# Kernel optimization log

Hardware: AMD Instinct MI355X
Metric: run time of the kernel (lower is better)

The kernel has to match this reference:

```python
import jax, jax.numpy as jnp
import numpy as np
import math

N = 100000
C = 128
E = 640000
ALPHA = 0.1
THETA = 1.0
LAYER = 4


def setup_inputs() -> dict:
    key = jax.random.key(0)
    k1, k2, k3, k4, k5, k6 = jax.random.split(key, 6)
    x = jax.random.normal(k1, (N, C), dtype=jnp.float32)
    x0 = jax.random.normal(k2, (N, C), dtype=jnp.float32)
    W = jax.random.normal(k3, (C, C), dtype=jnp.float32) / math.sqrt(C)
    b = jax.random.normal(k4, (C,), dtype=jnp.float32) * 0.01
    edge_index = jax.random.randint(k5, (2, E), 0, N, dtype=jnp.int64)
    return {"x": x, "x0": x0, "W": W, "b": b, "edge_index": edge_index}


def _symmetric_propagate(x, edge_index):
    n = x.shape[0]
    loop = jnp.arange(n, dtype=edge_index.dtype)
    src = jnp.concatenate([edge_index[0], loop])  # add self-loops (GCN norm)
    dst = jnp.concatenate([edge_index[1], loop])
    ones = jnp.ones(src.shape[0], dtype=x.dtype)
    deg = jax.ops.segment_sum(ones, dst, num_segments=n)
    dinv = jnp.where(deg > 0, jax.lax.rsqrt(deg), 0.0)
    norm = dinv[src] * dinv[dst]                  # [E+N]
    msgs = x[src] * norm[:, None]                 # gather + scale
    return jax.ops.segment_sum(msgs, dst, num_segments=n)  # scatter-add


def reference(x, x0, W, b, edge_index):
    propagated = _symmetric_propagate(x, edge_index)
    support = (1.0 - ALPHA) * propagated + ALPHA * x0
    beta = math.log(THETA / max(LAYER, 1) + 1.0)
    transformed = support @ W.T + b               # nn.Linear(channels, channels)
    return (1.0 - beta) * support + beta * transformed
```

## Files before the change

### kernel.cpp

```cpp
#include <hip/hip_runtime.h>
#include <stdint.h>

#define C 128
#define ALPHA_F 0.1f
#define ONE_MINUS_ALPHA 0.9f
#define BETA_F 0.22314355131420976f
#define ONE_MINUS_BETA 0.7768564486857902f
#define KSLOT 16

typedef __attribute__((ext_vector_type(8))) short bf16x8;
typedef __attribute__((ext_vector_type(4))) float f32x4;

__device__ inline float bf2f(unsigned short u) {
    union { unsigned int i; float f; } c;
    c.i = ((unsigned int)u) << 16;
    return c.f;
}
__device__ inline unsigned short f2bf(float f) {
    union { float f; unsigned int i; } c;
    c.f = f;
    unsigned int r = (c.i + 0x7FFFu + ((c.i >> 16) & 1u)) >> 16;
    return (unsigned short)r;
}

__global__ void k_init(const float* __restrict__ W, unsigned short* __restrict__ Vb,
                       int* __restrict__ cnt, int* __restrict__ ovf_cnt, int n) {
    int i = blockIdx.x * 256 + threadIdx.x;
    if (i == 0) *ovf_cnt = 0;
    if (i < n) cnt[i] = 0;
    if (i < C * C) {
        int j = i >> 7;
        int c = i & 127;
        float v = BETA_F * W[i] + ((j == c) ? ONE_MINUS_BETA : 0.f);
        Vb[i] = f2bf(v);
    }
}

__global__ void k_hist_place(const int* __restrict__ src, const int* __restrict__ dst,
                             int* __restrict__ cnt, int* __restrict__ sorted_src,
                             int* __restrict__ ovf_src, int* __restrict__ ovf_dst,
                             int* __restrict__ ovf_cnt, int e) {
    int i = blockIdx.x * blockDim.x + threadIdx.x;
    if (i < e) {
        int d = dst[i];
        int r = atomicAdd(&cnt[d], 1);
        if (r < KSLOT) {
            sorted_src[(size_t)d * KSLOT + r] = src[i];
        } else {
            int p = atomicAdd(ovf_cnt, 1);
            ovf_src[p] = src[i];
            ovf_dst[p] = d;
        }
    }
}

__global__ void k_ybf(const float* __restrict__ x, const int* __restrict__ cnt,
                      unsigned short* __restrict__ y, int n) {
    int t = blockIdx.x * 256 + threadIdx.x;
    int total = n * 32;
    if (t < total) {
        int i = t >> 5;
        float dv = rsqrtf((float)(cnt[i] + 1));
        float4 v = ((const float4*)x)[t];
        ushort4 o;
        o.x = f2bf(v.x * dv);
        o.y = f2bf(v.y * dv);
        o.z = f2bf(v.z * dv);
        o.w = f2bf(v.w * dv);
        ((ushort4*)y)[t] = o;
    }
}

__device__ __forceinline__ float4 acc_node(const ushort4* __restrict__ y4,
                                           int node, int len,
                                           int eidx, int l32, int base) {
    int m = (len < KSLOT) ? len : KSLOT;
    bool b1 = 1 < m, b2 = 2 < m, b3 = 3 < m;
    bool b4 = 4 < m, b5 = 5 < m, b6 = 6 < m, b7 = 7 < m;
    int s0 = __shfl(eidx, base + 0, 64);
    int s1 = __shfl(eidx, base + (b1 ? 1 : 0), 64);
    int s2 = __shfl(eidx, base + (b2 ? 2 : 0), 64);
    int s3 = __shfl(eidx, base + (b3 ? 3 : 0), 64);
    int s4 = __shfl(eidx, base + (b4 ? 4 : 0), 64);
    int s5 = __shfl(eidx, base + (b5 ? 5 : 0), 64);
    int s6 = __shfl(eidx, base + (b6 ? 6 : 0), 64);
    int s7 = __shfl(eidx, base + (b7 ? 7 : 0), 64);
    ushort4 v0 = y4[(size_t)s0 * 32 + l32];
    ushort4 v1 = y4[(size_t)s1 * 32 + l32];
    ushort4 v2 = y4[(size_t)s2 * 32 + l32];
    ushort4 v3 = y4[(size_t)s3 * 32 + l32];
    ushort4 v4 = y4[(size_t)s4 * 32 + l32];
    ushort4 v5 = y4[(size_t)s5 * 32 + l32];
    ushort4 v6 = y4[(size_t)s6 * 32 + l32];
    ushort4 v7 = y4[(size_t)s7 * 32 + l32];
    ushort4 vs = y4[(size_t)node * 32 + l32];

    float w0 = (0 < m) ? 1.f : 0.f, w1 = b1 ? 1.f : 0.f, w2 = b2 ? 1.f : 0.f, w3 = b3 ? 1.f : 0.f;
    float w4 = b4 ? 1.f : 0.f, w5 = b5 ? 1.f : 0.f, w6 = b6 ? 1.f : 0.f, w7 = b7 ? 1.f : 0.f;

    float4 acc;
    acc.x = bf2f(vs.x) + w0 * bf2f(v0.x) + w1 * bf2f(v1.x) + w2 * bf2f(v2.x) + w3 * bf2f(v3.x)
                       + w4 * bf2f(v4.x) + w5 * bf2f(v5.x) + w6 * bf2f(v6.x) + w7 * bf2f(v7.x);
    acc.y = bf2f(vs.y) + w0 * bf2f(v0.y) + w1 * bf2f(v1.y) + w2 * bf2f(v2.y) + w3 * bf2f(v3.y)
                       + w4 * bf2f(v4.y) + w5 * bf2f(v5.y) + w6 * bf2f(v6.y) + w7 * bf2f(v7.y);
    acc.z = bf2f(vs.z) + w0 * bf2f(v0.z) + w1 * bf2f(v1.z) + w2 * bf2f(v2.z) + w3 * bf2f(v3.z)
                       + w4 * bf2f(v4.z) + w5 * bf2f(v5.z) + w6 * bf2f(v6.z) + w7 * bf2f(v7.z);
    acc.w = bf2f(vs.w) + w0 * bf2f(v0.w) + w1 * bf2f(v1.w) + w2 * bf2f(v2.w) + w3 * bf2f(v3.w)
                       + w4 * bf2f(v4.w) + w5 * bf2f(v5.w) + w6 * bf2f(v6.w) + w7 * bf2f(v7.w);

    for (int j = 8; j < m; j += 4) {
        bool c1 = (j + 1) < m, c2 = (j + 2) < m, c3 = (j + 3) < m;
        int t0 = __shfl(eidx, base + j, 64);
        int t1 = __shfl(eidx, base + (c1 ? j + 1 : j), 64);
        int t2 = __shfl(eidx, base + (c2 ? j + 2 : j), 64);
        int t3 = __shfl(eidx, base + (c3 ? j + 3 : j), 64);
        ushort4 u0 = y4[(size_t)t0 * 32 + l32];
        ushort4 u1 = y4[(size_t)t1 * 32 + l32];
        ushort4 u2 = y4[(size_t)t2 * 32 + l32];
        ushort4 u3 = y4[(size_t)t3 * 32 + l32];
        float q1 = c1 ? 1.f : 0.f, q2 = c2 ? 1.f : 0.f, q3 = c3 ? 1.f : 0.f;
        acc.x += bf2f(u0.x) + q1 * bf2f(u1.x) + q2 * bf2f(u2.x) + q3 * bf2f(u3.x);
        acc.y += bf2f(u0.y) + q1 * bf2f(u1.y) + q2 * bf2f(u2.y) + q3 * bf2f(u3.y);
        acc.z += bf2f(u0.z) + q1 * bf2f(u1.z) + q2 * bf2f(u2.z) + q3 * bf2f(u3.z);
        acc.w += bf2f(u0.w) + q1 * bf2f(u1.w) + q2 * bf2f(u2.w) + q3 * bf2f(u3.w);
    }
    return acc;
}

__device__ __forceinline__ float4 add_ovf(float4 acc, const ushort4* __restrict__ y4,
                                          const int* __restrict__ ovf_src,
                                          const int* __restrict__ ovf_dst,
                                          int oc, int node, int l32) {
    for (int j = 0; j < oc; ++j) {
        if (ovf_dst[j] == node) {
            ushort4 u = y4[(size_t)ovf_src[j] * 32 + l32];
            acc.x += bf2f(u.x);
            acc.y += bf2f(u.y);
            acc.z += bf2f(u.z);
            acc.w += bf2f(u.w);
        }
    }
    return acc;
}

__global__ __launch_bounds__(256)
void k_gather(const unsigned short* __restrict__ y, const float* __restrict__ x0,
              const int* __restrict__ sorted_src, const int* __restrict__ cnt,
              const int* __restrict__ ovf_src, const int* __restrict__ ovf_dst,
              const int* __restrict__ ovf_cnt,
              float* __restrict__ soutf, unsigned short* __restrict__ soutb,
              int mode, int n) {
    int tid  = threadIdx.x;
    int l32  = tid & 31;
    int base = tid & 32;
    int hw   = tid >> 5;
    int node0 = blockIdx.x * 16 + hw * 2;
    if (node0 >= n) return;
    int node1 = node0 + 1;
    bool ok1 = node1 < n;
    int vn1 = ok1 ? node1 : node0;

    const ushort4* y4 = (const ushort4*)y;
    const f32x4* x04 = (const f32x4*)x0;

    int len0 = cnt[node0];
    int len1 = cnt[vn1];
    int m0 = (len0 < KSLOT) ? len0 : KSLOT;
    int m1 = (len1 < KSLOT) ? len1 : KSLOT;
    int e0 = (l32 < m0) ? sorted_src[(size_t)node0 * KSLOT + l32] : node0;
    int e1 = (l32 < m1) ? sorted_src[(size_t)vn1 * KSLOT + l32] : vn1;
    f32x4 xv0 = __builtin_nontemporal_load(x04 + (size_t)node0 * 32 + l32);
    f32x4 xv1 = __builtin_nontemporal_load(x04 + (size_t)vn1 * 32 + l32);

    float4 a0 = acc_node(y4, node0, len0, e0, l32, base);
    float4 a1 = acc_node(y4, vn1,   len1, e1, l32, base);

    if (len0 > KSLOT || len1 > KSLOT) {
        int oc = *ovf_cnt;
        if (len0 > KSLOT) a0 = add_ovf(a0, y4, ovf_src, ovf_dst, oc, node0, l32);
        if (len1 > KSLOT) a1 = add_ovf(a1, y4, ovf_src, ovf_dst, oc, vn1, l32);
    }

    float dv0 = rsqrtf((float)(len0 + 1));
    float dv1 = rsqrtf((float)(len1 + 1));

    float4 s0, s1;
    s0.x = ONE_MINUS_ALPHA * (dv0 * a0.x) + ALPHA_F * xv0.x;
    s0.y = ONE_MINUS_ALPHA * (dv0 * a0.y) + ALPHA_F * xv0.y;
    s0.z = ONE_MINUS_ALPHA * (dv0 * a0.z) + ALPHA_F * xv0.z;
    s0.w = ONE_MINUS_ALPHA * (dv0 * a0.w) + ALPHA_F * xv0.w;
    s1.x = ONE_MINUS_ALPHA * (dv1 * a1.x) + ALPHA_F * xv1.x;
    s1.y = ONE_MINUS_ALPHA * (dv1 * a1.y) + ALPHA_F * xv1.y;
    s1.z = ONE_MINUS_ALPHA * (dv1 * a1.z) + ALPHA_F * xv1.z;
    s1.w = ONE_MINUS_ALPHA * (dv1 * a1.w) + ALPHA_F * xv1.w;

    if (mode) {
        unsigned long long p0 =
            (unsigned long long)f2bf(s0.x)
          | ((unsigned long long)f2bf(s0.y) << 16)
          | ((unsigned long long)f2bf(s0.z) << 32)
          | ((unsigned long long)f2bf(s0.w) << 48);
        __builtin_nontemporal_store(
            p0, (unsigned long long*)(soutb + (size_t)node0 * C + l32 * 4));
        if (ok1) {
            unsigned long long p1 =
                (unsigned long long)f2bf(s1.x)
              | ((unsigned long long)f2bf(s1.y) << 16)
              | ((unsigned long long)f2bf(s1.z) << 32)
              | ((unsigned long long)f2bf(s1.w) << 48);
            __builtin_nontemporal_store(
                p1, (unsigned long long*)(soutb + (size_t)node1 * C + l32 * 4));
        }
    } else {
        ((float4*)soutf)[(size_t)node0 * 32 + l32] = s0;
        if (ok1) ((float4*)soutf)[(size_t)node1 * 32 + l32] = s1;
    }
}

__global__ __launch_bounds__(256)
void k_out(const float* __restrict__ sinf, const unsigned short* __restrict__ sinb,
           const unsigned short* __restrict__ Vb, const float* __restrict__ bias,
           float* __restrict__ out, int mode, int n) {
    __shared__ unsigned short wlds[128 * 128];

    int tid  = threadIdx.x;
    int row0 = blockIdx.x * 64;

    const uint4* Vb16 = (const uint4*)Vb;
    for (int i = tid; i < 2048; i += 256) {
        int j = i >> 4;
        int g = i & 15;
        uint4 v = Vb16[i];
        *(uint4*)&wlds[j * 128 + (g ^ (j & 7)) * 8] = v;
    }
    __syncthreads();

    int w    = tid >> 6;
    int lane = tid & 63;
    int l16  = lane & 15;
    int h    = lane >> 4;
    int arow = row0 + w * 16 + l16;
    int arow_c = (arow < n) ? arow : (n - 1);

    f32x4 acc[8];
    #pragma unroll
    for (int t = 0; t < 8; ++t) acc[t] = (f32x4){0.f, 0.f, 0.f, 0.f};

    #pragma unroll
    for (int k0 = 0; k0 < 128; k0 += 32) {
        bf16x8 a;
        if (mode) {
            a = *(const bf16x8*)(sinb + (size_t)arow_c * C + k0 + h * 8);
        } else {
            const float* ap = sinf + (size_t)arow_c * C + k0 + h * 8;
            float4 aa = *(const float4*)ap;
            float4 ab = *(const float4*)(ap + 4);
            union { unsigned short u[8]; bf16x8 v; } pk;
            pk.u[0] = f2bf(aa.x); pk.u[1] = f2bf(aa.y);
            pk.u[2] = f2bf(aa.z); pk.u[3] = f2bf(aa.w);
            pk.u[4] = f2bf(ab.x); pk.u[5] = f2bf(ab.y);
            pk.u[6] = f2bf(ab.z); pk.u[7] = f2bf(ab.w);
            a = pk.v;
        }
        #pragma unroll
        for (int t = 0; t < 8; ++t) {
            int brow = t * 16 + l16;
            int gb = ((k0 >> 3) + h) ^ (brow & 7);
            bf16x8 b = *(const bf16x8*)&wlds[brow * 128 + gb * 8];
            acc[t] = __builtin_amdgcn_mfma_f32_16x16x32_bf16(a, b, acc[t], 0, 0, 0);
        }
    }

    #pragma unroll
    for (int t = 0; t < 8; ++t) {
        int j  = t * 16 + l16;
        float bj = BETA_F * bias[j];
        #pragma unroll
        for (int e2 = 0; e2 < 4; ++e2) {
            int grow = row0 + w * 16 + h * 4 + e2;
            if (grow < n) {
                __builtin_nontemporal_store(acc[t][e2] + bj, &out[(size_t)grow * C + j]);
            }
        }
    }
}

extern "C" void kernel_launch(void* const* d_in, const int* in_sizes, int n_in,
                              void* d_out, int out_size, void* d_ws, size_t ws_size,
                              hipStream_t stream) {
    const float* x   = (const float*)d_in[0];
    const float* x0  = (const float*)d_in[1];
    const float* W   = (const float*)d_in[2];
    const float* b   = (const float*)d_in[3];
    const int*   ei  = (const int*)d_in[4];

    int n = in_sizes[0] / C;
    int e = in_sizes[4] / 2;
    const int* src = ei;
    const int* dst = ei + e;

    char* p = (char*)d_ws;
    auto alloc = [&](size_t bytes) {
        char* q = p;
        p += (bytes + 255) & ~(size_t)255;
        return q;
    };
    int* cnt        = (int*)alloc((size_t)n * 4);
    int* sorted_src = (int*)alloc((size_t)n * KSLOT * 4);
    int* ovf_src    = (int*)alloc((size_t)e * 4);
    int* ovf_dst    = (int*)alloc((size_t)e * 4);
    int* ovf_cnt    = (int*)alloc(256);
    unsigned short* Vb   = (unsigned short*)alloc((size_t)C * C * 2);
    unsigned short* y    = (unsigned short*)alloc((size_t)n * C * 2);
    unsigned short* sb16 = (unsigned short*)alloc((size_t)n * C * 2);

    size_t need = (size_t)(p - (char*)d_ws);
    int mode = (ws_size >= need) ? 1 : 0;

    float* out = (float*)d_out;

    int nb  = (n + 255) / 256;
    int eb  = (e + 255) / 256;
    int ybg = (n * 32 + 255) / 256;

    k_init      <<<nb, 256, 0, stream>>>(W, Vb, cnt, ovf_cnt, n);
    k_hist_place<<<eb, 256, 0, stream>>>(src, dst, cnt, sorted_src,
                                         ovf_src, ovf_dst, ovf_cnt, e);
    k_ybf       <<<ybg, 256, 0, stream>>>(x, cnt, y, n);
    k_gather    <<<(n + 15) / 16, 256, 0, stream>>>(y, x0, sorted_src, cnt,
                                                    ovf_src, ovf_dst, ovf_cnt,
                                                    out, sb16, mode, n);
    k_out       <<<(n + 63) / 64, 256, 0, stream>>>(out, sb16, Vb, b, out, mode, n);
}
```

Before: 115.5 us.

## Merge histogram placement and bf16 conversion; apply source degree scaling in gather

```diff
diff --git a/kernel.cpp b/kernel.cpp
--- a/kernel.cpp
+++ b/kernel.cpp
@@ -36,43 +36,44 @@
     }
 }
 
-__global__ void k_hist_place(const int* __restrict__ src, const int* __restrict__ dst,
-                             int* __restrict__ cnt, int* __restrict__ sorted_src,
-                             int* __restrict__ ovf_src, int* __restrict__ ovf_dst,
-                             int* __restrict__ ovf_cnt, int e) {
-    int i = blockIdx.x * blockDim.x + threadIdx.x;
-    if (i < e) {
-        int d = dst[i];
-        int r = atomicAdd(&cnt[d], 1);
-        if (r < KSLOT) {
-            sorted_src[(size_t)d * KSLOT + r] = src[i];
-        } else {
-            int p = atomicAdd(ovf_cnt, 1);
-            ovf_src[p] = src[i];
-            ovf_dst[p] = d;
-        }
-    }
-}
-
-__global__ void k_ybf(const float* __restrict__ x, const int* __restrict__ cnt,
-                      unsigned short* __restrict__ y, int n) {
-    int t = blockIdx.x * 256 + threadIdx.x;
-    int total = n * 32;
-    if (t < total) {
-        int i = t >> 5;
-        float dv = rsqrtf((float)(cnt[i] + 1));
-        float4 v = ((const float4*)x)[t];
-        ushort4 o;
-        o.x = f2bf(v.x * dv);
-        o.y = f2bf(v.y * dv);
-        o.z = f2bf(v.z * dv);
-        o.w = f2bf(v.w * dv);
-        ((ushort4*)y)[t] = o;
+__global__ void k_hp_ybf(const int* __restrict__ src, const int* __restrict__ dst,
+                         int* __restrict__ cnt, int* __restrict__ sorted_src,
+                         int* __restrict__ ovf_src, int* __restrict__ ovf_dst,
+                         int* __restrict__ ovf_cnt, int e,
+                         const float* __restrict__ x, unsigned short* __restrict__ y,
+                         int n, int eb) {
+    int bid = blockIdx.x;
+    if (bid < eb) {
+        int i = bid * 256 + threadIdx.x;
+        if (i < e) {
+            int d = dst[i];
+            int r = atomicAdd(&cnt[d], 1);
+            if (r < KSLOT) {
+                sorted_src[(size_t)d * KSLOT + r] = src[i];
+            } else {
+                int p = atomicAdd(ovf_cnt, 1);
+                ovf_src[p] = src[i];
+                ovf_dst[p] = d;
+            }
+        }
+    } else {
+        int t = (bid - eb) * 256 + threadIdx.x;
+        int total = n * 32;
+        if (t < total) {
+            float4 v = ((const float4*)x)[t];
+            ushort4 o;
+            o.x = f2bf(v.x);
+            o.y = f2bf(v.y);
+            o.z = f2bf(v.z);
+            o.w = f2bf(v.w);
+            ((ushort4*)y)[t] = o;
+        }
     }
 }
 
 __device__ __forceinline__ float4 acc_node(const ushort4* __restrict__ y4,
-                                           int node, int len,
+                                           const int* __restrict__ cnt,
+                                           int node, int len, float dv_self,
                                            int eidx, int l32, int base) {
     int m = (len < KSLOT) ? len : KSLOT;
     bool b1 = 1 < m, b2 = 2 < m, b3 = 3 < m;
@@ -94,50 +95,65 @@
     ushort4 v6 = y4[(size_t)s6 * 32 + l32];
     ushort4 v7 = y4[(size_t)s7 * 32 + l32];
     ushort4 vs = y4[(size_t)node * 32 + l32];
-
-    float w0 = (0 < m) ? 1.f : 0.f, w1 = b1 ? 1.f : 0.f, w2 = b2 ? 1.f : 0.f, w3 = b3 ? 1.f : 0.f;
-    float w4 = b4 ? 1.f : 0.f, w5 = b5 ? 1.f : 0.f, w6 = b6 ? 1.f : 0.f, w7 = b7 ? 1.f : 0.f;
+    int c0 = cnt[s0], c1 = cnt[s1], c2 = cnt[s2], c3 = cnt[s3];
+    int c4 = cnt[s4], c5 = cnt[s5], c6 = cnt[s6], c7 = cnt[s7];
+
+    float w0 = (0 < m) ? rsqrtf((float)(c0 + 1)) : 0.f;
+    float w1 = b1 ? rsqrtf((float)(c1 + 1)) : 0.f;
+    float w2 = b2 ? rsqrtf((float)(c2 + 1)) : 0.f;
+    float w3 = b3 ? rsqrtf((float)(c3 + 1)) : 0.f;
+    float w4 = b4 ? rsqrtf((float)(c4 + 1)) : 0.f;
+    float w5 = b5 ? rsqrtf((float)(c5 + 1)) : 0.f;
+    float w6 = b6 ? rsqrtf((float)(c6 + 1)) : 0.f;
+    float w7 = b7 ? rsqrtf((float)(c7 + 1)) : 0.f;
 
     float4 acc;
-    acc.x = bf2f(vs.x) + w0 * bf2f(v0.x) + w1 * bf2f(v1.x) + w2 * bf2f(v2.x) + w3 * bf2f(v3.x)
-                       + w4 * bf2f(v4.x) + w5 * bf2f(v5.x) + w6 * bf2f(v6.x) + w7 * bf2f(v7.x);
-    acc.y = bf2f(vs.y) + w0 * bf2f(v0.y) + w1 * bf2f(v1.y) + w2 * bf2f(v2.y) + w3 * bf2f(v3.y)
-                       + w4 * bf2f(v4.y) + w5 * bf2f(v5.y) + w6 * bf2f(v6.y) + w7 * bf2f(v7.y);
-    acc.z = bf2f(vs.z) + w0 * bf2f(v0.z) + w1 * bf2f(v1.z) + w2 * bf2f(v2.z) + w3 * bf2f(v3.z)
-                       + w4 * bf2f(v4.z) + w5 * bf2f(v5.z) + w6 * bf2f(v6.z) + w7 * bf2f(v7.z);
-    acc.w = bf2f(vs.w) + w0 * bf2f(v0.w) + w1 * bf2f(v1.w) + w2 * bf2f(v2.w) + w3 * bf2f(v3.w)
-                       + w4 * bf2f(v4.w) + w5 * bf2f(v5.w) + w6 * bf2f(v6.w) + w7 * bf2f(v7.w);
+    acc.x = dv_self * bf2f(vs.x) + w0 * bf2f(v0.x) + w1 * bf2f(v1.x) + w2 * bf2f(v2.x) + w3 * bf2f(v3.x)
+                                 + w4 * bf2f(v4.x) + w5 * bf2f(v5.x) + w6 * bf2f(v6.x) + w7 * bf2f(v7.x);
+    acc.y = dv_self * bf2f(vs.y) + w0 * bf2f(v0.y) + w1 * bf2f(v1.y) + w2 * bf2f(v2.y) + w3 * bf2f(v3.y)
+                                 + w4 * bf2f(v4.y) + w5 * bf2f(v5.y) + w6 * bf2f(v6.y) + w7 * bf2f(v7.y);
+    acc.z = dv_self * bf2f(vs.z) + w0 * bf2f(v0.z) + w1 * bf2f(v1.z) + w2 * bf2f(v2.z) + w3 * bf2f(v3.z)
+                                 + w4 * bf2f(v4.z) + w5 * bf2f(v5.z) + w6 * bf2f(v6.z) + w7 * bf2f(v7.z);
+    acc.w = dv_self * bf2f(vs.w) + w0 * bf2f(v0.w) + w1 * bf2f(v1.w) + w2 * bf2f(v2.w) + w3 * bf2f(v3.w)
+                                 + w4 * bf2f(v4.w) + w5 * bf2f(v5.w) + w6 * bf2f(v6.w) + w7 * bf2f(v7.w);
 
     for (int j = 8; j < m; j += 4) {
-        bool c1 = (j + 1) < m, c2 = (j + 2) < m, c3 = (j + 3) < m;
+        bool c1b = (j + 1) < m, c2b = (j + 2) < m, c3b = (j + 3) < m;
         int t0 = __shfl(eidx, base + j, 64);
-        int t1 = __shfl(eidx, base + (c1 ? j + 1 : j), 64);
-        int t2 = __shfl(eidx, base + (c2 ? j + 2 : j), 64);
-        int t3 = __shfl(eidx, base + (c3 ? j + 3 : j), 64);
+        int t1 = __shfl(eidx, base + (c1b ? j + 1 : j), 64);
+        int t2 = __shfl(eidx, base + (c2b ? j + 2 : j), 64);
+        int t3 = __shfl(eidx, base + (c3b ? j + 3 : j), 64);
         ushort4 u0 = y4[(size_t)t0 * 32 + l32];
         ushort4 u1 = y4[(size_t)t1 * 32 + l32];
         ushort4 u2 = y4[(size_t)t2 * 32 + l32];
         ushort4 u3 = y4[(size_t)t3 * 32 + l32];
-        float q1 = c1 ? 1.f : 0.f, q2 = c2 ? 1.f : 0.f, q3 = c3 ? 1.f : 0.f;
-        acc.x += bf2f(u0.x) + q1 * bf2f(u1.x) + q2 * bf2f(u2.x) + q3 * bf2f(u3.x);
-        acc.y += bf2f(u0.y) + q1 * bf2f(u1.y) + q2 * bf2f(u2.y) + q3 * bf2f(u3.y);
-        acc.z += bf2f(u0.z) + q1 * bf2f(u1.z) + q2 * bf2f(u2.z) + q3 * bf2f(u3.z);
-        acc.w += bf2f(u0.w) + q1 * bf2f(u1.w) + q2 * bf2f(u2.w) + q3 * bf2f(u3.w);
+        int d0 = cnt[t0], d1 = cnt[t1], d2 = cnt[t2], d3 = cnt[t3];
+        float q0 = rsqrtf((float)(d0 + 1));
+        float q1 = c1b ? rsqrtf((float)(d1 + 1)) : 0.f;
+        float q2 = c2b ? rsqrtf((float)(d2 + 1)) : 0.f;
+        float q3 = c3b ? rsqrtf((float)(d3 + 1)) : 0.f;
+        acc.x += q0 * bf2f(u0.x) + q1 * bf2f(u1.x) + q2 * bf2f(u2.x) + q3 * bf2f(u3.x);
+        acc.y += q0 * bf2f(u0.y) + q1 * bf2f(u1.y) + q2 * bf2f(u2.y) + q3 * bf2f(u3.y);
+        acc.z += q0 * bf2f(u0.z) + q1 * bf2f(u1.z) + q2 * bf2f(u2.z) + q3 * bf2f(u3.z);
+        acc.w += q0 * bf2f(u0.w) + q1 * bf2f(u1.w) + q2 * bf2f(u2.w) + q3 * bf2f(u3.w);
     }
     return acc;
 }
 
 __device__ __forceinline__ float4 add_ovf(float4 acc, const ushort4* __restrict__ y4,
+                                          const int* __restrict__ cnt,
                                           const int* __restrict__ ovf_src,
                                           const int* __restrict__ ovf_dst,
                                           int oc, int node, int l32) {
     for (int j = 0; j < oc; ++j) {
         if (ovf_dst[j] == node) {
-            ushort4 u = y4[(size_t)ovf_src[j] * 32 + l32];
-            acc.x += bf2f(u.x);
-            acc.y += bf2f(u.y);
-            acc.z += bf2f(u.z);
-            acc.w += bf2f(u.w);
+            int s = ovf_src[j];
+            float wv = rsqrtf((float)(cnt[s] + 1));
+            ushort4 u = y4[(size_t)s * 32 + l32];
+            acc.x += wv * bf2f(u.x);
+            acc.y += wv * bf2f(u.y);
+            acc.z += wv * bf2f(u.z);
+            acc.w += wv * bf2f(u.w);
         }
     }
     return acc;
@@ -172,17 +188,17 @@
     f32x4 xv0 = __builtin_nontemporal_load(x04 + (size_t)node0 * 32 + l32);
     f32x4 xv1 = __builtin_nontemporal_load(x04 + (size_t)vn1 * 32 + l32);
 
-    float4 a0 = acc_node(y4, node0, len0, e0, l32, base);
-    float4 a1 = acc_node(y4, vn1,   len1, e1, l32, base);
+    float dv0 = rsqrtf((float)(len0 + 1));
+    float dv1 = rsqrtf((float)(len1 + 1));
+
+    float4 a0 = acc_node(y4, cnt, node0, len0, dv0, e0, l32, base);
+    float4 a1 = acc_node(y4, cnt, vn1,   len1, dv1, e1, l32, base);
 
     if (len0 > KSLOT || len1 > KSLOT) {
         int oc = *ovf_cnt;
-        if (len0 > KSLOT) a0 = add_ovf(a0, y4, ovf_src, ovf_dst, oc, node0, l32);
-        if (len1 > KSLOT) a1 = add_ovf(a1, y4, ovf_src, ovf_dst, oc, vn1, l32);
-    }
-
-    float dv0 = rsqrtf((float)(len0 + 1));
-    float dv1 = rsqrtf((float)(len1 + 1));
+        if (len0 > KSLOT) a0 = add_ovf(a0, y4, cnt, ovf_src, ovf_dst, oc, node0, l32);
+        if (len1 > KSLOT) a1 = add_ovf(a1, y4, cnt, ovf_src, ovf_dst, oc, vn1, l32);
+    }
 
     float4 s0, s1;
     s0.x = ONE_MINUS_ALPHA * (dv0 * a0.x) + ALPHA_F * xv0.x;
@@ -323,12 +339,12 @@
     int eb  = (e + 255) / 256;
     int ybg = (n * 32 + 255) / 256;
 
-    k_init      <<<nb, 256, 0, stream>>>(W, Vb, cnt, ovf_cnt, n);
-    k_hist_place<<<eb, 256, 0, stream>>>(src, dst, cnt, sorted_src,
-                                         ovf_src, ovf_dst, ovf_cnt, e);
-    k_ybf       <<<ybg, 256, 0, stream>>>(x, cnt, y, n);
-    k_gather    <<<(n + 15) / 16, 256, 0, stream>>>(y, x0, sorted_src, cnt,
-                                                    ovf_src, ovf_dst, ovf_cnt,
-                                                    out, sb16, mode, n);
-    k_out       <<<(n + 63) / 64, 256, 0, stream>>>(out, sb16, Vb, b, out, mode, n);
-}
+    k_init   <<<nb, 256, 0, stream>>>(W, Vb, cnt, ovf_cnt, n);
+    k_hp_ybf <<<eb + ybg, 256, 0, stream>>>(src, dst, cnt, sorted_src,
+                                            ovf_src, ovf_dst, ovf_cnt, e,
+                                            x, y, n, eb);
+    k_gather <<<(n + 15) / 16, 256, 0, stream>>>(y, x0, sorted_src, cnt,
+                                                 ovf_src, ovf_dst, ovf_cnt,
+                                                 out, sb16, mode, n);
+    k_out    <<<(n + 63) / 64, 256, 0, stream>>>(out, sb16, Vb, b, out, mode, n);
+}
```

After: 118.6 us. 1.03x slower.
